# Kernel optimization log

Hardware: AMD Instinct MI355X
Metric: run time of the kernel (lower is better)

## Reference

```python
import jax, jax.numpy as jnp
import numpy as np

B, N, P, E = 64, 512, 256, 4096          # batch, nodes (stations), partition nodes, edges
NUM_NWP, LP, F = 8, 16, 32               # num_nwp, local_points, local_cnn_dims
NT, ED, H, W = 8, 8, 64, 8               # num_temp, edge_feature_dims, decf_mlp_hidden, weight_function_dim
G, RH = 64, 256                          # gnn_dim, readout_hid_dim
H1, Q = 128, 9                           # mlp_hid_dim1, num quantiles


def setup_inputs() -> dict:
    key = jax.random.key(0)
    ks = iter(jax.random.split(key, 40))
    def rn(shape, s=0.05):
        return jax.random.normal(next(ks), shape, dtype=jnp.float32) * s
    # one-hot incidence matrices: each edge has one left (partition) node and one right node
    lidx = jax.random.randint(next(ks), (E,), 0, P)
    ridx = jax.random.randint(next(ks), (E,), 0, N)
    linc = jnp.zeros((P, E), jnp.float32).at[lidx, jnp.arange(E)].set(1.0)
    rinc = jnp.zeros((E, N), jnp.float32).at[jnp.arange(E), ridx].set(1.0)
    inp = {
        "x1": jax.random.normal(next(ks), (B, NUM_NWP * N, LP), dtype=jnp.float32),
        "x2": jax.random.normal(next(ks), (B, NT), dtype=jnp.float32),
        # LocalConv1D grouped conv (torch OIW layout: [Cout, Cin/groups, K])
        "conv_w": rn((F * N, NUM_NWP, LP)), "conv_b": rn((F * N,)),
        # WDSGCN2 edge-weight MLP
        "k1_w": rn((H, ED)), "k1_b": rn((H,)),
        "k2_w": rn((H, NT)),
        "k3_w": rn((H, F)),
        "k4_w": rn((H, F)),
        "k5_w": rn((W, H)), "k5_b": rn((W,)),
        "gc_w": rn((G, F * W)), "gc_b": rn((G,)),
        # readout
        "r0_w": rn((RH, G * P)),
        "r1_w": rn((RH, NT)), "r1_b": rn((RH,)),
        "r2_w": rn((RH, P)),
        "r3_w": rn((P, RH)), "r3_b": rn((P,)),
        # SMlp (forward uses l1 -> ELU -> l3 only)
        "l1_w": rn((H1, NT + G)), "l1_b": rn((H1,)),
        "l3_w": rn((Q, H1)), "l3_b": rn((Q,)),
        # buffers
        "ef": jax.random.normal(next(ks), (E, ED + 1), dtype=jnp.float32),
        "linc": linc,
        "rinc": rinc,
        "cap_feature": jax.random.normal(next(ks), (P,), dtype=jnp.float32),
        "partition_idx": jnp.arange(P, dtype=jnp.int32) * (N // P),
    }
    return inp


def reference(x1, x2, conv_w, conv_b, k1_w, k1_b, k2_w, k3_w, k4_w, k5_w, k5_b,
              gc_w, gc_b, r0_w, r1_w, r1_b, r2_w, r3_w, r3_b,
              l1_w, l1_b, l3_w, l3_b, ef, linc, rinc, cap_feature, partition_idx):
    b = x1.shape[0]
    # --- LocalConv1D: grouped conv1d (valid padding, output length 1) + ReLU ---
    y = jax.lax.conv_general_dilated(x1, conv_w, (1,), 'VALID',
                                     dimension_numbers=('NCH', 'OIH', 'NCH'),
                                     feature_group_count=N)
    x = jax.nn.relu(y + conv_b[None, :, None]).reshape(b, N, F)      # [B,N,F]
    # --- WDSGCN2: per-edge weight kernel ---
    kern = ef[:, :-1] @ k1_w.T + k1_b                                # [E,H]
    kern = kern[None] + (x2 @ k2_w.T)[:, None, :]                    # [B,E,H]
    xp = x[:, partition_idx, :]                                      # [B,P,F]
    kern = kern + jnp.einsum('pe,bpf->bef', linc, xp) @ k3_w.T       # left-node feats
    rx = jnp.einsum('en,bnf->bef', rinc, x)                          # right-node feats [B,E,F]
    kern = kern + rx @ k4_w.T
    kern = jax.nn.relu(jax.nn.leaky_relu(kern, 0.02) @ k5_w.T + k5_b)  # [B,E,W]
    # --- message = kernel (outer) right-node features, aggregated by left incidence ---
    msg = kern[:, :, :, None] * rx[:, :, None, :]                    # [B,E,W,F]
    agg = jnp.einsum('pe,bewf->bpwf', linc, msg).reshape(b, P, W * F)
    yg = jax.nn.relu(agg @ gc_w.T + gc_b)                            # [B,P,G]
    # --- readout attention over partition nodes ---
    h = yg.reshape(b, -1) @ r0_w.T + (x2 @ r1_w.T + r1_b) + cap_feature @ r2_w.T
    wt = jax.nn.relu(jax.nn.leaky_relu(h, 0.01) @ r3_w.T + r3_b)     # [B,P]
    res = jnp.einsum('bp,bpg->bg', wt, yg)                           # [B,G]
    # --- SMlp head ---
    z = jnp.concatenate([res, x2], axis=1)
    z = jax.nn.elu(z @ l1_w.T + l1_b)
    return z @ l3_w.T + l3_b                                         # [B,Q]
```

## Files before the change

kernel.cpp:

```cpp
#include <hip/hip_runtime.h>
#include <math.h>

#define B_ 64
#define N_ 512
#define P_ 256
#define E_ 4096
#define F_ 32
#define H_ 64
#define W_ 8
#define G_ 64
#define RH_ 256

#define X_OFF   0
#define T4_OFF  (X_OFF + N_*B_*F_)
#define T3_OFF  (T4_OFF + N_*B_*H_)
#define KB_OFF  (T3_OFF + P_*B_*H_)
#define KW_OFF  (KB_OFF + E_*H_)
#define YG_OFF  (KW_OFF + E_*B_*W_)
#define HB_OFF  (YG_OFF + B_*P_*G_)
#define RES_OFF (HB_OFF + B_*RH_)
#define INT_OFF (RES_OFF + 4*B_*G_)

__device__ __forceinline__ unsigned short f2bf(float f) {
  unsigned int u = __float_as_uint(f);
  u = u + 0x7fffu + ((u >> 16) & 1u);
  return (unsigned short)(u >> 16);
}

__global__ __launch_bounds__(256) void k_dc(
    const float* __restrict__ linc, const float* __restrict__ rinc,
    int* __restrict__ lidx, int* __restrict__ ridx,
    const float* __restrict__ x1, const float* __restrict__ conv_w,
    const float* __restrict__ conv_b, float* __restrict__ x,
    unsigned short* __restrict__ xh,
    const float* __restrict__ cap, const float* __restrict__ r2_w,
    float* __restrict__ capv) {
  __shared__ float wsm[32 * 132];
  __shared__ float xsm[8192];
  int blk = blockIdx.x, t = threadIdx.x;
  if (blk < 3072) {
    int i4 = blk * 256 + t;
    const int L4 = (P_ * E_) / 4;
    if (i4 < L4) {
      float4 v = ((const float4*)linc)[i4];
      int i = i4 * 4;
      int p = i >> 12, e = i & 4095;
      if (v.x != 0.0f) lidx[e]     = p;
      if (v.y != 0.0f) lidx[e + 1] = p;
      if (v.z != 0.0f) lidx[e + 2] = p;
      if (v.w != 0.0f) lidx[e + 3] = p;
    } else {
      int j4 = i4 - L4;
      float4 v = ((const float4*)rinc)[j4];
      int j = j4 * 4;
      int e = j >> 9, n = j & 511;
      if (v.x != 0.0f) ridx[e] = n;
      if (v.y != 0.0f) ridx[e] = n + 1;
      if (v.z != 0.0f) ridx[e] = n + 2;
      if (v.w != 0.0f) ridx[e] = n + 3;
    }
    return;
  }
  if (blk == 3584) {
    float acc = 0.0f;
    const float* rr = r2_w + t * 256;
    for (int p4 = 0; p4 < 64; p4++) {
      float4 cv = ((const float4*)cap)[p4];
      float4 rv = ((const float4*)rr)[p4];
      acc += cv.x * rv.x + cv.y * rv.y + cv.z * rv.z + cv.w * rv.w;
    }
    capv[t] = acc;
    return;
  }
  int n = blk - 3072;
  for (int i = t; i < 1024; i += 256) {
    int f = i >> 5, j = i & 31;
    ((float4*)wsm)[f * 33 + j] = ((const float4*)(conv_w + n * 4096))[i];
  }
  for (int i = t; i < 2048; i += 256) {
    int b = i >> 5, j = i & 31;
    ((float4*)xsm)[i] = ((const float4*)(x1 + b * 65536 + n * 128))[j];
  }
  __syncthreads();
  int f = t & 31, bq = t >> 5;
  float cb = conv_b[n * 32 + f];
  float acc[8];
#pragma unroll
  for (int bi = 0; bi < 8; bi++) acc[bi] = cb;
  const float4* wf4 = (const float4*)wsm + f * 33;
  const float4* xb4 = (const float4*)xsm + bq * 256;
#pragma unroll 4
  for (int k4 = 0; k4 < 32; k4++) {
    float4 wv = wf4[k4];
#pragma unroll
    for (int bi = 0; bi < 8; bi++) {
      float4 xv = xb4[bi * 32 + k4];
      acc[bi] += wv.x * xv.x + wv.y * xv.y + wv.z * xv.z + wv.w * xv.w;
    }
  }
#pragma unroll
  for (int bi = 0; bi < 8; bi++) {
    int b = bq * 8 + bi;
    float vv = fmaxf(acc[bi], 0.0f);
    x[n * 2048 + b * 32 + f] = vv;
    xh[n * 2048 + b * 32 + f] = f2bf(vv);
  }
}

__global__ __launch_bounds__(256) void k_prep(
    const float* __restrict__ x, const int* __restrict__ pidx,
    const float* __restrict__ k3_w, const float* __restrict__ k4_w,
    const float* __restrict__ x2, const float* __restrict__ k2_w,
    const float* __restrict__ ef, const float* __restrict__ k1_w,
    const float* __restrict__ k1_b,
    const float* __restrict__ r1_w, const float* __restrict__ r1_b,
    const float* __restrict__ capv,
    const int* __restrict__ lidx, const int* __restrict__ ridx,
    unsigned short* __restrict__ t4h, float* __restrict__ t3,
    float* __restrict__ kb, float* __restrict__ hbuf,
    int* __restrict__ part_start, int2* __restrict__ pe2) {
  __shared__ float xsh[2048];
  __shared__ float wsh[64 * 36];
  __shared__ float x2s[512];
  __shared__ float k2s[512];
  __shared__ int cnt[256];
  __shared__ int buf[256];
  __shared__ int cur[256];
  int blk = blockIdx.x, t = threadIdx.x;
  if (blk < 768) {
    bool isT4 = blk < 512;
    int n = isT4 ? blk : pidx[blk - 512];
    const float* wmat = isT4 ? k4_w : k3_w;
    float* outp = t3 + (isT4 ? 0 : (blk - 512) * 4096);
    for (int i = t; i < 512; i += 256) {
      ((float4*)xsh)[i] = ((const float4*)(x + n * 2048))[i];
      int h = i >> 3, j = i & 7;
      ((float4*)wsh)[h * 9 + j] = ((const float4*)wmat)[i];
    }
    if (isT4) {
      for (int i = t; i < 128; i += 256) {
        ((float4*)x2s)[i] = ((const float4*)x2)[i];
        ((float4*)k2s)[i] = ((const float4*)k2_w)[i];
      }
    }
    __syncthreads();
    int h = t & 63, bq = t >> 6;
    float wreg[32];
#pragma unroll
    for (int j = 0; j < 8; j++) {
      float4 v = ((float4*)wsh)[h * 9 + j];
      wreg[4 * j] = v.x; wreg[4 * j + 1] = v.y; wreg[4 * j + 2] = v.z; wreg[4 * j + 3] = v.w;
    }
    float w2[8];
    if (isT4) {
      float4 u = ((float4*)k2s)[h * 2], v = ((float4*)k2s)[h * 2 + 1];
      w2[0] = u.x; w2[1] = u.y; w2[2] = u.z; w2[3] = u.w;
      w2[4] = v.x; w2[5] = v.y; w2[6] = v.z; w2[7] = v.w;
    }
    for (int bi = 0; bi < 16; bi++) {
      int b = bq * 16 + bi;
      float acc = 0.0f;
#pragma unroll
      for (int j = 0; j < 8; j++) {
        float4 xv = ((float4*)xsh)[b * 8 + j];
        acc += xv.x * wreg[4 * j] + xv.y * wreg[4 * j + 1] +
               xv.z * wreg[4 * j + 2] + xv.w * wreg[4 * j + 3];
      }
      if (isT4) {
        float4 u = ((float4*)x2s)[b * 2], v = ((float4*)x2s)[b * 2 + 1];
        acc += u.x * w2[0] + u.y * w2[1] + u.z * w2[2] + u.w * w2[3] +
               v.x * w2[4] + v.y * w2[5] + v.z * w2[6] + v.w * w2[7];
        t4h[blk * 4096 + b * 64 + h] = f2bf(acc);
      } else {
        outp[b * 64 + h] = acc;
      }
    }
  } else if (blk < 1792) {
    int o = (blk - 768) * 256 + t;
    int e = o >> 6, h = o & 63;
    float acc = k1_b[h];
    const float* er = ef + e * 9;
    const float* kr = k1_w + h * 8;
#pragma unroll
    for (int d = 0; d < 8; d++) acc += er[d] * kr[d];
    kb[o] = acc;
  } else if (blk < 1856) {
    int o = (blk - 1792) * 256 + t;
    int rh = o & 255;
    float acc = r1_b[rh] + capv[rh];
    const float* xr = x2 + (o >> 8) * 8;
    const float* rr = r1_w + rh * 8;
#pragma unroll
    for (int d = 0; d < 8; d++) acc += xr[d] * rr[d];
    hbuf[o] = acc;
  } else {
    cnt[t] = 0;
    __syncthreads();
    for (int e = t; e < E_; e += 256) atomicAdd(&cnt[lidx[e]], 1);
    __syncthreads();
    buf[t] = cnt[t];
    __syncthreads();
    for (int off = 1; off < 256; off <<= 1) {
      int add = (t >= off) ? buf[t - off] : 0;
      __syncthreads();
      buf[t] += add;
      __syncthreads();
    }
    part_start[t + 1] = buf[t];
    if (t == 0) part_start[0] = 0;
    cur[t] = buf[t] - cnt[t];
    __syncthreads();
    for (int e = t; e < E_; e += 256) {
      int p = lidx[e];
      int pos = atomicAdd(&cur[p], 1);
      pe2[pos] = make_int2(e | (p << 16), ridx[e]);
    }
  }
}

__global__ __launch_bounds__(256) void k_kern(
    const float* __restrict__ kb, const float* __restrict__ t3,
    const unsigned short* __restrict__ t4h, const float* __restrict__ k5_w,
    const float* __restrict__ k5_b, const int2* __restrict__ pe2,
    float* __restrict__ kv) {
  __shared__ float k5t[4 * 520];
  int bid = blockIdx.x;
  int pos = (bid & 7) * 512 + (bid >> 3);
  int t = threadIdx.x;
  for (int i = t; i < 512; i += 256) {
    int h = i >> 3, w = i & 7;
    float v = k5_w[w * 64 + h];
#pragma unroll
    for (int qq = 0; qq < 4; qq++) k5t[qq * 520 + i] = v;
  }
  int2 c = pe2[pos];
  int e = c.x & 0xffff, p = c.x >> 16, r = c.y;
  int s = t & 3, b = t >> 2;
  __syncthreads();
  const float* kq = k5t + s * 520 + s * 128;
  const float4* kb4 = (const float4*)(kb + e * 64 + s * 16);
  const float4* t34 = (const float4*)(t3 + p * 4096 + b * 64 + s * 16);
  const int4* t4p = (const int4*)(t4h + r * 4096 + b * 64 + s * 16);
  int4 ta = t4p[0], tb = t4p[1];
  float t4v[16];
  {
    unsigned int uu;
    uu = (unsigned int)ta.x; t4v[0]  = __uint_as_float(uu << 16); t4v[1]  = __uint_as_float(uu & 0xffff0000u);
    uu = (unsigned int)ta.y; t4v[2]  = __uint_as_float(uu << 16); t4v[3]  = __uint_as_float(uu & 0xffff0000u);
    uu = (unsigned int)ta.z; t4v[4]  = __uint_as_float(uu << 16); t4v[5]  = __uint_as_float(uu & 0xffff0000u);
    uu = (unsigned int)ta.w; t4v[6]  = __uint_as_float(uu << 16); t4v[7]  = __uint_as_float(uu & 0xffff0000u);
    uu = (unsigned int)tb.x; t4v[8]  = __uint_as_float(uu << 16); t4v[9]  = __uint_as_float(uu & 0xffff0000u);
    uu = (unsigned int)tb.y; t4v[10] = __uint_as_float(uu << 16); t4v[11] = __uint_as_float(uu & 0xffff0000u);
    uu = (unsigned int)tb.z; t4v[12] = __uint_as_float(uu << 16); t4v[13] = __uint_as_float(uu & 0xffff0000u);
    uu = (unsigned int)tb.w; t4v[14] = __uint_as_float(uu << 16); t4v[15] = __uint_as_float(uu & 0xffff0000u);
  }
  float lk[16];
#pragma unroll
  for (int j4 = 0; j4 < 4; j4++) {
    float4 a = kb4[j4], cc = t34[j4];
    float v;
    v = a.x + cc.x + t4v[j4 * 4 + 0]; lk[j4 * 4 + 0] = v > 0.0f ? v : 0.02f * v;
    v = a.y + cc.y + t4v[j4 * 4 + 1]; lk[j4 * 4 + 1] = v > 0.0f ? v : 0.02f * v;
    v = a.z + cc.z + t4v[j4 * 4 + 2]; lk[j4 * 4 + 2] = v > 0.0f ? v : 0.02f * v;
    v = a.w + cc.w + t4v[j4 * 4 + 3]; lk[j4 * 4 + 3] = v > 0.0f ? v : 0.02f * v;
  }
  float pw[8] = {0, 0, 0, 0, 0, 0, 0, 0};
#pragma unroll
  for (int j = 0; j < 16; j++) {
    float4 u = *(const float4*)(kq + j * 8);
    float4 v = *(const float4*)(kq + j * 8 + 4);
    float l = lk[j];
    pw[0] += l * u.x; pw[1] += l * u.y; pw[2] += l * u.z; pw[3] += l * u.w;
    pw[4] += l * v.x; pw[5] += l * v.y; pw[6] += l * v.z; pw[7] += l * v.w;
  }
#pragma unroll
  for (int w = 0; w < 8; w++) {
    pw[w] += __shfl_xor(pw[w], 1);
    pw[w] += __shfl_xor(pw[w], 2);
  }
  float2 o;
  o.x = fmaxf(pw[2 * s] + k5_b[2 * s], 0.0f);
  o.y = fmaxf(pw[2 * s + 1] + k5_b[2 * s + 1], 0.0f);
  *(float2*)(kv + pos * 512 + b * 8 + 2 * s) = o;
}

__global__ __launch_bounds__(512, 2) void k_agg(
    const unsigned short* __restrict__ xh, const float* __restrict__ kv,
    const int2* __restrict__ pe2, const int* __restrict__ part_start,
    const float* __restrict__ gc_w, const float* __restrict__ gc_b,
    float* __restrict__ yg) {
  __shared__ float accS[64 * 128];
  __shared__ float gcS[64 * 256];
  int p = blockIdx.x, t = threadIdx.x;
  int slot = t >> 8;
  int ts = t & 255;
  int s = ts & 3, b = ts >> 2;
  for (int i4 = t; i4 < 4096; i4 += 512)
    ((float4*)gcS)[i4] = ((const float4*)gc_w)[i4];
  float acc[64];
#pragma unroll
  for (int j = 0; j < 64; j++) acc[j] = 0.0f;
  int s0 = part_start[p], s1 = part_start[p + 1];
  int idx = s0 + slot;
  int r = (idx < s1) ? pe2[idx].y : 0;
  for (; idx < s1; idx += 2) {
    int rn = (idx + 2 < s1) ? pe2[idx + 2].y : 0;
    const float4* kvp = (const float4*)(kv + idx * 512 + b * 8);
    float4 ka = kvp[0], kc = kvp[1];
    int4 xw = *(const int4*)(xh + r * 2048 + b * 32 + s * 8);
    float kw[8] = {ka.x, ka.y, ka.z, ka.w, kc.x, kc.y, kc.z, kc.w};
    float xa[8];
    {
      unsigned int uu;
      uu = (unsigned int)xw.x; xa[0] = __uint_as_float(uu << 16); xa[1] = __uint_as_float(uu & 0xffff0000u);
      uu = (unsigned int)xw.y; xa[2] = __uint_as_float(uu << 16); xa[3] = __uint_as_float(uu & 0xffff0000u);
      uu = (unsigned int)xw.z; xa[4] = __uint_as_float(uu << 16); xa[5] = __uint_as_float(uu & 0xffff0000u);
      uu = (unsigned int)xw.w; xa[6] = __uint_as_float(uu << 16); xa[7] = __uint_as_float(uu & 0xffff0000u);
    }
#pragma unroll
    for (int w = 0; w < 8; w++)
#pragma unroll
      for (int j = 0; j < 8; j++) acc[w * 8 + j] += kw[w] * xa[j];
    r = rn;
  }
  int gq = t >> 6, be = t & 63;
  float ac[8];
#pragma unroll
  for (int i = 0; i < 8; i++) ac[i] = 0.0f;
#pragma unroll
  for (int ph = 0; ph < 2; ph++) {
    if (ph) __syncthreads();
    if (slot == 0) {
#pragma unroll
      for (int w2 = 0; w2 < 4; w2++)
#pragma unroll
        for (int j4 = 0; j4 < 2; j4++) {
          int khalf4 = w2 * 8 + s * 2 + j4;
          int phys4 = (khalf4 & 24) | ((khalf4 ^ b) & 7);
          int j = (ph * 4 + w2) * 8 + j4 * 4;
          *(float4*)(accS + b * 128 + phys4 * 4) =
              make_float4(acc[j], acc[j + 1], acc[j + 2], acc[j + 3]);
        }
    }
    __syncthreads();
    if (slot == 1) {
#pragma unroll
      for (int w2 = 0; w2 < 4; w2++)
#pragma unroll
        for (int j4 = 0; j4 < 2; j4++) {
          int khalf4 = w2 * 8 + s * 2 + j4;
          int phys4 = (khalf4 & 24) | ((khalf4 ^ b) & 7);
          int j = (ph * 4 + w2) * 8 + j4 * 4;
          float4* ptr = (float4*)(accS + b * 128 + phys4 * 4);
          float4 o = *ptr;
          o.x += acc[j]; o.y += acc[j + 1]; o.z += acc[j + 2]; o.w += acc[j + 3];
          *ptr = o;
        }
    }
    __syncthreads();
    for (int k4h = 0; k4h < 32; k4h++) {
      int phys4 = (k4h & 24) | ((k4h ^ be) & 7);
      float4 av = *(const float4*)(accS + be * 128 + phys4 * 4);
      int w2 = k4h >> 3;
      int k4g = (ph * 4 + w2) * 8 + (k4h & 7);
#pragma unroll
      for (int i = 0; i < 8; i++) {
        float4 wv = *(const float4*)(gcS + (gq * 8 + i) * 256 + k4g * 4);
        ac[i] += av.x * wv.x + av.y * wv.y + av.z * wv.z + av.w * wv.w;
      }
    }
  }
  float* yp = yg + be * 16384 + p * 64 + gq * 8;
#pragma unroll
  for (int i = 0; i < 8; i++)
    yp[i] = fmaxf(ac[i] + gc_b[gq * 8 + i], 0.0f);
}

__global__ __launch_bounds__(256) void k_r0(const float* __restrict__ yg,
    const float* __restrict__ r0_w, float* __restrict__ part) {
  __shared__ float ygs[64 * 68];
  __shared__ float wts[64 * 68];
  int bid = blockIdx.x, t = threadIdx.x;
  int kc = ((bid >> 5) << 3) | (bid & 7);
  int rhq = (bid >> 3) & 3;
  int rh0 = rhq * 64;
  int lane = t & 63, wv = t >> 6;
  int b4 = lane & 15;
  int r4 = (lane >> 4) | (wv << 2);
  float acc[4][4];
#pragma unroll
  for (int i = 0; i < 4; i++)
#pragma unroll
    for (int j = 0; j < 4; j++) acc[i][j] = 0.0f;
  for (int sub = 0; sub < 4; sub++) {
    int k0 = kc * 256 + sub * 64;
    if (sub) __syncthreads();
    {
      int rl = t >> 2, kq = t & 3;
      const float* src = r0_w + (rh0 + rl) * 16384 + k0 + kq * 16;
#pragma unroll
      for (int u = 0; u < 4; u++) {
        float4 v = *(const float4*)(src + u * 4);
        int kk = kq * 16 + u * 4;
        wts[(kk + 0) * 68 + rl] = v.x;
        wts[(kk + 1) * 68 + rl] = v.y;
        wts[(kk + 2) * 68 + rl] = v.z;
        wts[(kk + 3) * 68 + rl] = v.w;
      }
    }
    {
      int b = t >> 2, kq = t & 3;
      const float* src = yg + b * 16384 + k0 + kq * 16;
#pragma unroll
      for (int u = 0; u < 4; u++) {
        float4 v = *(const float4*)(src + u * 4);
        int kk = kq * 16 + u * 4;
        ygs[(kk + 0) * 68 + b] = v.x;
        ygs[(kk + 1) * 68 + b] = v.y;
        ygs[(kk + 2) * 68 + b] = v.z;
        ygs[(kk + 3) * 68 + b] = v.w;
      }
    }
    __syncthreads();
    const float* yp = ygs + b4 * 4;
    const float* wp = wts + r4 * 4;
#pragma unroll 4
    for (int k = 0; k < 64; k++) {
      float4 yv = *(const float4*)(yp + k * 68);
      float4 wr = *(const float4*)(wp + k * 68);
      float ya[4] = {yv.x, yv.y, yv.z, yv.w};
      float wa[4] = {wr.x, wr.y, wr.z, wr.w};
#pragma unroll
      for (int i = 0; i < 4; i++)
#pragma unroll
        for (int j = 0; j < 4; j++) acc[i][j] += ya[i] * wa[j];
    }
  }
  float* pb = part + kc * 16384 + rh0 + r4 * 4;
#pragma unroll
  for (int i = 0; i < 4; i++) {
    *(float4*)(pb + (b4 * 4 + i) * 256) =
        make_float4(acc[i][0], acc[i][1], acc[i][2], acc[i][3]);
  }
}

__global__ __launch_bounds__(256) void k_r0red(const float* __restrict__ part,
    float* __restrict__ hbuf) {
  int blk = blockIdx.x;
  int oq = blk & 63, kq = blk >> 6;
  int o = oq * 256 + threadIdx.x;
  float s = 0.0f;
  const float* pp = part + kq * 16 * 16384 + o;
#pragma unroll 8
  for (int kc = 0; kc < 16; kc++) s += pp[kc * 16384];
  atomicAdd(&hbuf[o], s);
}

__global__ __launch_bounds__(256) void k_wt_res(const float* __restrict__ hbuf,
    const float* __restrict__ r3_w, const float* __restrict__ r3_b,
    const float* __restrict__ yg, float* __restrict__ res4) {
  __shared__ float hs[256];
  __shared__ float wts[64];
  __shared__ float red[256];
  int blk = blockIdx.x;
  int bb = blk >> 2, pq = blk & 3;
  int t = threadIdx.x;
  float hv = hbuf[bb * 256 + t];
  hs[t] = hv > 0.0f ? hv : 0.01f * hv;
  __syncthreads();
  int pl = t >> 2, c = t & 3;
  int pp = pq * 64 + pl;
  const float4* wrow = (const float4*)(r3_w + pp * 256 + c * 64);
  const float4* h4 = (const float4*)(hs) + c * 16;
  float a = 0.0f;
#pragma unroll
  for (int j = 0; j < 16; j++) {
    float4 w4 = wrow[j], hh = h4[j];
    a += hh.x * w4.x + hh.y * w4.y + hh.z * w4.z + hh.w * w4.w;
  }
  a += __shfl_xor(a, 1);
  a += __shfl_xor(a, 2);
  if (c == 0) wts[pl] = fmaxf(a + r3_b[pp], 0.0f);
  __syncthreads();
  int g = t & 63, ch = t >> 6;
  float r = 0.0f;
  const float* ygp = yg + bb * 16384 + pq * 4096 + g;
#pragma unroll
  for (int pi = 0; pi < 16; pi++) {
    int pl2 = ch * 16 + pi;
    r += wts[pl2] * ygp[pl2 * 64];
  }
  red[t] = r;
  __syncthreads();
  if (t < 64)
    res4[pq * 4096 + bb * 64 + t] = red[t] + red[t + 64] + red[t + 128] + red[t + 192];
}

__global__ __launch_bounds__(128) void k_final(const float* __restrict__ res4,
    const float* __restrict__ x2, const float* __restrict__ l1_w,
    const float* __restrict__ l1_b, const float* __restrict__ l3_w,
    const float* __restrict__ l3_b, float* __restrict__ out) {
  __shared__ float zs[128];
  int bb = blockIdx.x, t = threadIdx.x;
  float acc = l1_b[t];
  const float* wrow = l1_w + t * 72;
  const float* rr = res4 + bb * 64;
#pragma unroll 8
  for (int j = 0; j < 64; j++) {
    float rv = rr[j] + rr[4096 + j] + rr[8192 + j] + rr[12288 + j];
    acc += rv * wrow[j];
  }
  const float* xr = x2 + bb * 8;
#pragma unroll
  for (int j = 0; j < 8; j++) acc += xr[j] * wrow[64 + j];
  zs[t] = acc > 0.0f ? acc : expm1f(acc);
  __syncthreads();
  if (t < 9) {
    float o = l3_b[t];
    const float* w3 = l3_w + t * 128;
    for (int j = 0; j < 128; j++) o += zs[j] * w3[j];
    out[bb * 9 + t] = o;
  }
}

extern "C" void kernel_launch(void* const* d_in, const int* in_sizes, int n_in,
                              void* d_out, int out_size, void* d_ws, size_t ws_size,
                              hipStream_t stream) {
  (void)in_sizes; (void)n_in; (void)out_size; (void)ws_size;
  const float* x1     = (const float*)d_in[0];
  const float* x2     = (const float*)d_in[1];
  const float* conv_w = (const float*)d_in[2];
  const float* conv_b = (const float*)d_in[3];
  const float* k1_w   = (const float*)d_in[4];
  const float* k1_b   = (const float*)d_in[5];
  const float* k2_w   = (const float*)d_in[6];
  const float* k3_w   = (const float*)d_in[7];
  const float* k4_w   = (const float*)d_in[8];
  const float* k5_w   = (const float*)d_in[9];
  const float* k5_b   = (const float*)d_in[10];
  const float* gc_w   = (const float*)d_in[11];
  const float* gc_b   = (const float*)d_in[12];
  const float* r0_w   = (const float*)d_in[13];
  const float* r1_w   = (const float*)d_in[14];
  const float* r1_b   = (const float*)d_in[15];
  const float* r2_w   = (const float*)d_in[16];
  const float* r3_w   = (const float*)d_in[17];
  const float* r3_b   = (const float*)d_in[18];
  const float* l1_w   = (const float*)d_in[19];
  const float* l1_b   = (const float*)d_in[20];
  const float* l3_w   = (const float*)d_in[21];
  const float* l3_b   = (const float*)d_in[22];
  const float* ef     = (const float*)d_in[23];
  const float* linc   = (const float*)d_in[24];
  const float* rinc   = (const float*)d_in[25];
  const float* cap    = (const float*)d_in[26];
  const int*   pidx   = (const int*)d_in[27];
  float* out = (float*)d_out;

  float* ws   = (float*)d_ws;
  float* xbuf = ws + X_OFF;
  unsigned short* t4h = (unsigned short*)(ws + T4_OFF);
  unsigned short* xh  = (unsigned short*)(ws + T4_OFF + N_*B_*H_/2);
  float* t3   = ws + T3_OFF;
  float* kb   = ws + KB_OFF;
  float* kv   = ws + KW_OFF;
  float* yg   = ws + YG_OFF;
  float* hbuf = ws + HB_OFF;
  float* res4 = ws + RES_OFF;
  float* part = ws + X_OFF;
  int* ib = (int*)(ws + INT_OFF);
  int* lidx = ib;
  int* ridx = ib + 4096;
  int* part_start = ib + 8192;
  int2* pe2 = (int2*)(ib + 8704);
  float* capv = ws + INT_OFF + 16896;

  hipLaunchKernelGGL(k_dc, dim3(3585), dim3(256), 0, stream,
                     linc, rinc, lidx, ridx, x1, conv_w, conv_b, xbuf, xh,
                     cap, r2_w, capv);
  hipLaunchKernelGGL(k_prep, dim3(1857), dim3(256), 0, stream,
                     xbuf, pidx, k3_w, k4_w, x2, k2_w, ef, k1_w, k1_b,
                     r1_w, r1_b, capv, lidx, ridx,
                     t4h, t3, kb, hbuf, part_start, pe2);
  hipLaunchKernelGGL(k_kern, dim3(4096), dim3(256), 0, stream,
                     kb, t3, t4h, k5_w, k5_b, pe2, kv);
  hipLaunchKernelGGL(k_agg, dim3(256), dim3(512), 0, stream,
                     xh, kv, pe2, part_start, gc_w, gc_b, yg);
  hipLaunchKernelGGL(k_r0, dim3(256), dim3(256), 0, stream, yg, r0_w, part);
  hipLaunchKernelGGL(k_r0red, dim3(256), dim3(256), 0, stream, part, hbuf);
  hipLaunchKernelGGL(k_wt_res, dim3(256), dim3(256), 0, stream, hbuf, r3_w, r3_b, yg, res4);
  hipLaunchKernelGGL(k_final, dim3(64), dim3(128), 0, stream,
                     res4, x2, l1_w, l1_b, l3_w, l3_b, out);
}
```

Before: 229.2 us.

## Fuse readout tail kernels into one and process four edges per k_kern block

The partial-sum reduction, attention weight, weighted readout and SMlp head were three separate kernels; they become one kernel with one block per batch row. This removes two launches, the atomicAdd into hbuf and the res4 round trip through global memory. In exchange the tail runs on only 64 blocks, each doing a serial 64-step reduction over part. Separately, k_kern now handles four edge positions per block, so the shared k5 weight staging is paid once per four edges and the grid shrinks from 4096 to 1024 blocks.

```diff
diff --git a/kernel.cpp b/kernel.cpp
--- a/kernel.cpp
+++ b/kernel.cpp
@@ -225,7 +225,6 @@
     float* __restrict__ kv) {
   __shared__ float k5t[4 * 520];
   int bid = blockIdx.x;
-  int pos = (bid & 7) * 512 + (bid >> 3);
   int t = threadIdx.x;
   for (int i = t; i < 512; i += 256) {
     int h = i >> 3, w = i & 7;
@@ -233,55 +232,60 @@
 #pragma unroll
     for (int qq = 0; qq < 4; qq++) k5t[qq * 520 + i] = v;
   }
-  int2 c = pe2[pos];
-  int e = c.x & 0xffff, p = c.x >> 16, r = c.y;
   int s = t & 3, b = t >> 2;
   __syncthreads();
   const float* kq = k5t + s * 520 + s * 128;
-  const float4* kb4 = (const float4*)(kb + e * 64 + s * 16);
-  const float4* t34 = (const float4*)(t3 + p * 4096 + b * 64 + s * 16);
-  const int4* t4p = (const int4*)(t4h + r * 4096 + b * 64 + s * 16);
-  int4 ta = t4p[0], tb = t4p[1];
-  float t4v[16];
-  {
-    unsigned int uu;
-    uu = (unsigned int)ta.x; t4v[0]  = __uint_as_float(uu << 16); t4v[1]  = __uint_as_float(uu & 0xffff0000u);
-    uu = (unsigned int)ta.y; t4v[2]  = __uint_as_float(uu << 16); t4v[3]  = __uint_as_float(uu & 0xffff0000u);
-    uu = (unsigned int)ta.z; t4v[4]  = __uint_as_float(uu << 16); t4v[5]  = __uint_as_float(uu & 0xffff0000u);
-    uu = (unsigned int)ta.w; t4v[6]  = __uint_as_float(uu << 16); t4v[7]  = __uint_as_float(uu & 0xffff0000u);
-    uu = (unsigned int)tb.x; t4v[8]  = __uint_as_float(uu << 16); t4v[9]  = __uint_as_float(uu & 0xffff0000u);
-    uu = (unsigned int)tb.y; t4v[10] = __uint_as_float(uu << 16); t4v[11] = __uint_as_float(uu & 0xffff0000u);
-    uu = (unsigned int)tb.z; t4v[12] = __uint_as_float(uu << 16); t4v[13] = __uint_as_float(uu & 0xffff0000u);
-    uu = (unsigned int)tb.w; t4v[14] = __uint_as_float(uu << 16); t4v[15] = __uint_as_float(uu & 0xffff0000u);
-  }
-  float lk[16];
-#pragma unroll
-  for (int j4 = 0; j4 < 4; j4++) {
-    float4 a = kb4[j4], cc = t34[j4];
-    float v;
-    v = a.x + cc.x + t4v[j4 * 4 + 0]; lk[j4 * 4 + 0] = v > 0.0f ? v : 0.02f * v;
-    v = a.y + cc.y + t4v[j4 * 4 + 1]; lk[j4 * 4 + 1] = v > 0.0f ? v : 0.02f * v;
-    v = a.z + cc.z + t4v[j4 * 4 + 2]; lk[j4 * 4 + 2] = v > 0.0f ? v : 0.02f * v;
-    v = a.w + cc.w + t4v[j4 * 4 + 3]; lk[j4 * 4 + 3] = v > 0.0f ? v : 0.02f * v;
-  }
-  float pw[8] = {0, 0, 0, 0, 0, 0, 0, 0};
-#pragma unroll
-  for (int j = 0; j < 16; j++) {
-    float4 u = *(const float4*)(kq + j * 8);
-    float4 v = *(const float4*)(kq + j * 8 + 4);
-    float l = lk[j];
-    pw[0] += l * u.x; pw[1] += l * u.y; pw[2] += l * u.z; pw[3] += l * u.w;
-    pw[4] += l * v.x; pw[5] += l * v.y; pw[6] += l * v.z; pw[7] += l * v.w;
-  }
-#pragma unroll
-  for (int w = 0; w < 8; w++) {
-    pw[w] += __shfl_xor(pw[w], 1);
-    pw[w] += __shfl_xor(pw[w], 2);
-  }
-  float2 o;
-  o.x = fmaxf(pw[2 * s] + k5_b[2 * s], 0.0f);
-  o.y = fmaxf(pw[2 * s + 1] + k5_b[2 * s + 1], 0.0f);
-  *(float2*)(kv + pos * 512 + b * 8 + 2 * s) = o;
+  float kb5_0 = k5_b[2 * s], kb5_1 = k5_b[2 * s + 1];
+  int pos0 = (bid & 7) * 512 + (bid >> 3) * 4;
+  for (int j = 0; j < 4; j++) {
+    int pos = pos0 + j;
+    int2 c = pe2[pos];
+    int e = c.x & 0xffff, p = c.x >> 16, r = c.y;
+    const float4* kb4 = (const float4*)(kb + e * 64 + s * 16);
+    const float4* t34 = (const float4*)(t3 + p * 4096 + b * 64 + s * 16);
+    const int4* t4p = (const int4*)(t4h + r * 4096 + b * 64 + s * 16);
+    int4 ta = t4p[0], tb = t4p[1];
+    float t4v[16];
+    {
+      unsigned int uu;
+      uu = (unsigned int)ta.x; t4v[0]  = __uint_as_float(uu << 16); t4v[1]  = __uint_as_float(uu & 0xffff0000u);
+      uu = (unsigned int)ta.y; t4v[2]  = __uint_as_float(uu << 16); t4v[3]  = __uint_as_float(uu & 0xffff0000u);
+      uu = (unsigned int)ta.z; t4v[4]  = __uint_as_float(uu << 16); t4v[5]  = __uint_as_float(uu & 0xffff0000u);
+      uu = (unsigned int)ta.w; t4v[6]  = __uint_as_float(uu << 16); t4v[7]  = __uint_as_float(uu & 0xffff0000u);
+      uu = (unsigned int)tb.x; t4v[8]  = __uint_as_float(uu << 16); t4v[9]  = __uint_as_float(uu & 0xffff0000u);
+      uu = (unsigned int)tb.y; t4v[10] = __uint_as_float(uu << 16); t4v[11] = __uint_as_float(uu & 0xffff0000u);
+      uu = (unsigned int)tb.z; t4v[12] = __uint_as_float(uu << 16); t4v[13] = __uint_as_float(uu & 0xffff0000u);
+      uu = (unsigned int)tb.w; t4v[14] = __uint_as_float(uu << 16); t4v[15] = __uint_as_float(uu & 0xffff0000u);
+    }
+    float lk[16];
+#pragma unroll
+    for (int j4 = 0; j4 < 4; j4++) {
+      float4 a = kb4[j4], cc = t34[j4];
+      float v;
+      v = a.x + cc.x + t4v[j4 * 4 + 0]; lk[j4 * 4 + 0] = v > 0.0f ? v : 0.02f * v;
+      v = a.y + cc.y + t4v[j4 * 4 + 1]; lk[j4 * 4 + 1] = v > 0.0f ? v : 0.02f * v;
+      v = a.z + cc.z + t4v[j4 * 4 + 2]; lk[j4 * 4 + 2] = v > 0.0f ? v : 0.02f * v;
+      v = a.w + cc.w + t4v[j4 * 4 + 3]; lk[j4 * 4 + 3] = v > 0.0f ? v : 0.02f * v;
+    }
+    float pw[8] = {0, 0, 0, 0, 0, 0, 0, 0};
+#pragma unroll
+    for (int jj = 0; jj < 16; jj++) {
+      float4 u = *(const float4*)(kq + jj * 8);
+      float4 v = *(const float4*)(kq + jj * 8 + 4);
+      float l = lk[jj];
+      pw[0] += l * u.x; pw[1] += l * u.y; pw[2] += l * u.z; pw[3] += l * u.w;
+      pw[4] += l * v.x; pw[5] += l * v.y; pw[6] += l * v.z; pw[7] += l * v.w;
+    }
+#pragma unroll
+    for (int w = 0; w < 8; w++) {
+      pw[w] += __shfl_xor(pw[w], 1);
+      pw[w] += __shfl_xor(pw[w], 2);
+    }
+    float2 o;
+    o.x = fmaxf(pw[2 * s] + kb5_0, 0.0f);
+    o.y = fmaxf(pw[2 * s + 1] + kb5_1, 0.0f);
+    *(float2*)(kv + pos * 512 + b * 8 + 2 * s) = o;
+  }
 }
 
 __global__ __launch_bounds__(512, 2) void k_agg(
@@ -444,76 +448,62 @@
   }
 }
 
-__global__ __launch_bounds__(256) void k_r0red(const float* __restrict__ part,
-    float* __restrict__ hbuf) {
-  int blk = blockIdx.x;
-  int oq = blk & 63, kq = blk >> 6;
-  int o = oq * 256 + threadIdx.x;
-  float s = 0.0f;
-  const float* pp = part + kq * 16 * 16384 + o;
+__global__ __launch_bounds__(256) void k_tail(
+    const float* __restrict__ hbuf, const float* __restrict__ part,
+    const float* __restrict__ r3_w, const float* __restrict__ r3_b,
+    const float* __restrict__ yg, const float* __restrict__ x2,
+    const float* __restrict__ l1_w, const float* __restrict__ l1_b,
+    const float* __restrict__ l3_w, const float* __restrict__ l3_b,
+    float* __restrict__ out) {
+  __shared__ float hs[256];
+  __shared__ float wts[256];
+  __shared__ float red[256];
+  __shared__ float res[64];
+  __shared__ float zs[128];
+  int bb = blockIdx.x, t = threadIdx.x;
+  float hv = hbuf[bb * 256 + t];
+  const float* pp = part + bb * 256 + t;
 #pragma unroll 8
-  for (int kc = 0; kc < 16; kc++) s += pp[kc * 16384];
-  atomicAdd(&hbuf[o], s);
-}
-
-__global__ __launch_bounds__(256) void k_wt_res(const float* __restrict__ hbuf,
-    const float* __restrict__ r3_w, const float* __restrict__ r3_b,
-    const float* __restrict__ yg, float* __restrict__ res4) {
-  __shared__ float hs[256];
-  __shared__ float wts[64];
-  __shared__ float red[256];
-  int blk = blockIdx.x;
-  int bb = blk >> 2, pq = blk & 3;
-  int t = threadIdx.x;
-  float hv = hbuf[bb * 256 + t];
+  for (int kc = 0; kc < 64; kc++) hv += pp[kc * 16384];
   hs[t] = hv > 0.0f ? hv : 0.01f * hv;
   __syncthreads();
   int pl = t >> 2, c = t & 3;
-  int pp = pq * 64 + pl;
-  const float4* wrow = (const float4*)(r3_w + pp * 256 + c * 64);
   const float4* h4 = (const float4*)(hs) + c * 16;
-  float a = 0.0f;
-#pragma unroll
-  for (int j = 0; j < 16; j++) {
-    float4 w4 = wrow[j], hh = h4[j];
-    a += hh.x * w4.x + hh.y * w4.y + hh.z * w4.z + hh.w * w4.w;
-  }
-  a += __shfl_xor(a, 1);
-  a += __shfl_xor(a, 2);
-  if (c == 0) wts[pl] = fmaxf(a + r3_b[pp], 0.0f);
+  for (int pq = 0; pq < 4; pq++) {
+    int p = pq * 64 + pl;
+    const float4* wrow = (const float4*)(r3_w + p * 256 + c * 64);
+    float a = 0.0f;
+#pragma unroll
+    for (int j = 0; j < 16; j++) {
+      float4 w4 = wrow[j], hh = h4[j];
+      a += hh.x * w4.x + hh.y * w4.y + hh.z * w4.z + hh.w * w4.w;
+    }
+    a += __shfl_xor(a, 1);
+    a += __shfl_xor(a, 2);
+    if (c == 0) wts[p] = fmaxf(a + r3_b[p], 0.0f);
+  }
   __syncthreads();
   int g = t & 63, ch = t >> 6;
   float r = 0.0f;
-  const float* ygp = yg + bb * 16384 + pq * 4096 + g;
-#pragma unroll
-  for (int pi = 0; pi < 16; pi++) {
-    int pl2 = ch * 16 + pi;
-    r += wts[pl2] * ygp[pl2 * 64];
+  const float* ygp = yg + bb * 16384 + g;
+  for (int pi = 0; pi < 64; pi++) {
+    int p2 = ch * 64 + pi;
+    r += wts[p2] * ygp[p2 * 64];
   }
   red[t] = r;
   __syncthreads();
-  if (t < 64)
-    res4[pq * 4096 + bb * 64 + t] = red[t] + red[t + 64] + red[t + 128] + red[t + 192];
-}
-
-__global__ __launch_bounds__(128) void k_final(const float* __restrict__ res4,
-    const float* __restrict__ x2, const float* __restrict__ l1_w,
-    const float* __restrict__ l1_b, const float* __restrict__ l3_w,
-    const float* __restrict__ l3_b, float* __restrict__ out) {
-  __shared__ float zs[128];
-  int bb = blockIdx.x, t = threadIdx.x;
-  float acc = l1_b[t];
-  const float* wrow = l1_w + t * 72;
-  const float* rr = res4 + bb * 64;
+  if (t < 64) res[t] = red[t] + red[t + 64] + red[t + 128] + red[t + 192];
+  __syncthreads();
+  if (t < 128) {
+    float acc = l1_b[t];
+    const float* wrow = l1_w + t * 72;
 #pragma unroll 8
-  for (int j = 0; j < 64; j++) {
-    float rv = rr[j] + rr[4096 + j] + rr[8192 + j] + rr[12288 + j];
-    acc += rv * wrow[j];
-  }
-  const float* xr = x2 + bb * 8;
-#pragma unroll
-  for (int j = 0; j < 8; j++) acc += xr[j] * wrow[64 + j];
-  zs[t] = acc > 0.0f ? acc : expm1f(acc);
+    for (int j = 0; j < 64; j++) acc += res[j] * wrow[j];
+    const float* xr = x2 + bb * 8;
+#pragma unroll
+    for (int j = 0; j < 8; j++) acc += xr[j] * wrow[64 + j];
+    zs[t] = acc > 0.0f ? acc : expm1f(acc);
+  }
   __syncthreads();
   if (t < 9) {
     float o = l3_b[t];
@@ -566,7 +556,6 @@
   float* kv   = ws + KW_OFF;
   float* yg   = ws + YG_OFF;
   float* hbuf = ws + HB_OFF;
-  float* res4 = ws + RES_OFF;
   float* part = ws + X_OFF;
   int* ib = (int*)(ws + INT_OFF);
   int* lidx = ib;
@@ -582,13 +571,11 @@
                      xbuf, pidx, k3_w, k4_w, x2, k2_w, ef, k1_w, k1_b,
                      r1_w, r1_b, capv, lidx, ridx,
                      t4h, t3, kb, hbuf, part_start, pe2);
-  hipLaunchKernelGGL(k_kern, dim3(4096), dim3(256), 0, stream,
+  hipLaunchKernelGGL(k_kern, dim3(1024), dim3(256), 0, stream,
                      kb, t3, t4h, k5_w, k5_b, pe2, kv);
   hipLaunchKernelGGL(k_agg, dim3(256), dim3(512), 0, stream,
                      xh, kv, pe2, part_start, gc_w, gc_b, yg);
   hipLaunchKernelGGL(k_r0, dim3(256), dim3(256), 0, stream, yg, r0_w, part);
-  hipLaunchKernelGGL(k_r0red, dim3(256), dim3(256), 0, stream, part, hbuf);
-  hipLaunchKernelGGL(k_wt_res, dim3(256), dim3(256), 0, stream, hbuf, r3_w, r3_b, yg, res4);
-  hipLaunchKernelGGL(k_final, dim3(64), dim3(128), 0, stream,
-                     res4, x2, l1_w, l1_b, l3_w, l3_b, out);
-}
+  hipLaunchKernelGGL(k_tail, dim3(64), dim3(256), 0, stream,
+                     hbuf, part, r3_w, r3_b, yg, x2, l1_w, l1_b, l3_w, l3_b, out);
+}
```

Result: slower. 234.3 us (+2.2%).
